# Optimization experiments

Measured on AMD Instinct MI355X. Metric: run time of the kernel, lower is better.

The kernel has to match this reference:

```python
import jax, jax.numpy as jnp
import numpy as np

B, D, H = 4096, 66, 512  # batch, system dim (22 atoms * 3), MLP hidden


def _dynamics(t, xs, W1, b1, W2, b2, W3, b3):
    # CNF vector field f(t, x): 3-layer SiLU MLP on concat([x, t])
    h = jnp.concatenate([xs, t], axis=1)          # [B, D+1]
    h = jax.nn.silu(h @ W1 + b1)                  # [B, H]
    h = jax.nn.silu(h @ W2 + b2)                  # [B, H]
    return h @ W3 + b3                            # [B, D]


def setup_inputs() -> dict:
    key = jax.random.key(0)
    ks = jax.random.split(key, 5)
    xs = jax.random.normal(ks[0], (B, D), dtype=jnp.float32)
    t = jax.random.uniform(ks[1], (B, 1), dtype=jnp.float32)
    W1 = jax.random.normal(ks[2], (D + 1, H), dtype=jnp.float32) / np.float32(np.sqrt(D + 1))
    b1 = jnp.zeros((H,), dtype=jnp.float32)
    W2 = jax.random.normal(ks[3], (H, H), dtype=jnp.float32) / np.float32(np.sqrt(H))
    b2 = jnp.zeros((H,), dtype=jnp.float32)
    W3 = jax.random.normal(ks[4], (H, D), dtype=jnp.float32) / np.float32(np.sqrt(H))
    b3 = jnp.zeros((D,), dtype=jnp.float32)
    return {"xs": xs, "t": t, "W1": W1, "b1": b1, "W2": W2, "b2": b2, "W3": W3, "b3": b3}


def reference(xs, t, W1, b1, W2, b2, W3, b3):
    # Exact divergence: trace of Jacobian d f / d x, computed with D JVPs
    # (forward-mode equivalent of the torch per-dim autograd.grad loop).
    def f(x):
        return _dynamics(t, x, W1, b1, W2, b2, W3, b3)

    dxs = f(xs)                                   # [B, D]
    eye = jnp.eye(D, dtype=xs.dtype)              # basis vectors e_i

    def jvp_col(e):
        _, tang = jax.jvp(f, (xs,), (jnp.broadcast_to(e, xs.shape),))
        return tang                               # J @ e_i, shape [B, D]

    tangs = jax.vmap(jvp_col)(eye)                # [D, B, D]
    div = jnp.einsum('dbd->b', tangs)             # sum_i (J e_i)_i = tr(J)
    return dxs, -div[:, None]
```

## Files before the change

kernel.cpp:

```cpp
#include <hip/hip_runtime.h>

#define Bn 4096
#define Dn 66
#define Hn 512

typedef __attribute__((ext_vector_type(8))) short short8;
typedef __attribute__((ext_vector_type(4))) float f32x4;

__device__ __forceinline__ unsigned short f2bf(float x) {
    union { float f; unsigned u; } v; v.f = x;
    unsigned r = v.u + 0x7fffu + ((v.u >> 16) & 1u);
    return (unsigned short)(r >> 16);
}
__device__ __forceinline__ float bf2f(unsigned short h) {
    union { float f; unsigned u; } v; v.u = ((unsigned)h) << 16; return v.f;
}


__global__ __launch_bounds__(512, 2) void k_pack(
    const float* __restrict__ W1, const float* __restrict__ W2,
    const float* __restrict__ W3,
    unsigned short* __restrict__ W2P, unsigned short* __restrict__ CmP,
    unsigned short* __restrict__ W3P)
{
    const int bid = blockIdx.x, tid = threadIdx.x;
    const int lane = tid & 63, wv = tid >> 6;

    if (bid < 64) {
        const int tix = bid*8 + wv;
        const int ks = tix & 15;
        const int n = lane & 15, kg = lane >> 4;
        const int c = (tix >> 4)*16 + n;
        const int abase = ks*32 + kg*8;
        float w2v[8], m[8];
        #pragma unroll
        for (int j = 0; j < 8; ++j) {
            w2v[j] = W2[(size_t)(abase + j)*Hn + c];
            m[j] = 0.f;
        }
        for (int i = 0; i < Dn; ++i) {
            const float w3 = W3[(size_t)c*Dn + i];
            const float4 w1a = *(const float4*)&W1[(size_t)i*Hn + abase];
            const float4 w1b = *(const float4*)&W1[(size_t)i*Hn + abase + 4];
            m[0] = fmaf(w3, w1a.x, m[0]); m[1] = fmaf(w3, w1a.y, m[1]);
            m[2] = fmaf(w3, w1a.z, m[2]); m[3] = fmaf(w3, w1a.w, m[3]);
            m[4] = fmaf(w3, w1b.x, m[4]); m[5] = fmaf(w3, w1b.y, m[5]);
            m[6] = fmaf(w3, w1b.z, m[6]); m[7] = fmaf(w3, w1b.w, m[7]);
        }
        short8 pw, pc;
        #pragma unroll
        for (int j = 0; j < 8; ++j) {
            pw[j] = (short)f2bf(w2v[j]);
            pc[j] = (short)f2bf(w2v[j] * m[j]);
        }
        const size_t off = ((size_t)tix*64 + lane)*8;
        *(short8*)&W2P[off] = pw;
        *(short8*)&CmP[off] = pc;
    } else {
        const int tix = (bid - 64)*8 + wv;
        if (tix < 80) {
            const int ks = tix & 15;
            const int n = lane & 15, kg = lane >> 4;
            const int j_out = (tix >> 4)*16 + n;
            const int abase = ks*32 + kg*8;
            short8 p;
            #pragma unroll
            for (int j = 0; j < 8; ++j)
                p[j] = (j_out < Dn) ? (short)f2bf(W3[(size_t)(abase + j)*Dn + j_out]) : (short)0;
            *(short8*)&W3P[((size_t)tix*64 + lane)*8] = p;
        }
    }
}

__global__ __launch_bounds__(512, 2) void k_main(
    const float* __restrict__ xs, const float* __restrict__ tt,
    const float* __restrict__ W1, const float* __restrict__ b1,
    const unsigned short* __restrict__ W2P, const unsigned short* __restrict__ CmP,
    const float* __restrict__ b2,
    const unsigned short* __restrict__ W3P, const float* __restrict__ b3,
    float* __restrict__ out)
{
    __shared__ __align__(16) unsigned short sA[3*8192];
    __shared__ __align__(16) unsigned short sH[8192];
    __shared__ __align__(16) unsigned short sL[8192];
    __shared__ float sX[67*16];
    __shared__ float sRed[8*16];

    const int tid = threadIdx.x, lane = tid & 63, wv = tid >> 6;
    const int rt = blockIdx.x, r0 = rt*16;
    const int n = lane & 15, kg = lane >> 4;

    for (int idx = tid; idx < 67*16; idx += 512) {
        const int i = idx >> 4, r = idx & 15;
        sX[idx] = (i < Dn) ? xs[(size_t)(r0+r)*Dn + i] : tt[r0+r];
    }
    __syncthreads();

    {
        const int rg = lane & 7, cg = lane >> 3;
        const int cA = wv*64 + cg*4, cB = cA + 32;
        float z[2][8];
        {
            const float4 bA4 = *(const float4*)&b1[cA];
            const float4 bB4 = *(const float4*)&b1[cB];
            const float bb[8] = {bA4.x,bA4.y,bA4.z,bA4.w, bB4.x,bB4.y,bB4.z,bB4.w};
            #pragma unroll
            for (int j = 0; j < 8; ++j) { z[0][j] = bb[j]; z[1][j] = bb[j]; }
        }
        for (int i = 0; i < 67; ++i) {
            const float2 xf = *(const float2*)&sX[i*16 + 2*rg];
            const float4 wA = *(const float4*)&W1[(size_t)i*Hn + cA];
            const float4 wB = *(const float4*)&W1[(size_t)i*Hn + cB];
            const float ww[8] = {wA.x,wA.y,wA.z,wA.w, wB.x,wB.y,wB.z,wB.w};
            #pragma unroll
            for (int j = 0; j < 8; ++j) {
                z[0][j] = fmaf(xf.x, ww[j], z[0][j]);
                z[1][j] = fmaf(xf.y, ww[j], z[1][j]);
            }
        }
        const int kgrp = cg >> 1, joff = (cg & 1)*4;
        #pragma unroll
        for (int rr = 0; rr < 2; ++rr) {
            const int r = 2*rg + rr;
            #pragma unroll
            for (int grp = 0; grp < 2; ++grp) {
                ushort4 phi, plo, ps;
                unsigned short* PH = (unsigned short*)&phi;
                unsigned short* PL = (unsigned short*)&plo;
                unsigned short* PS = (unsigned short*)&ps;
                #pragma unroll
                for (int j = 0; j < 4; ++j) {
                    const float zv = z[rr][grp*4 + j];
                    const float sg = 1.f / (1.f + __expf(-zv));
                    const float h  = zv * sg;
                    const float sp = sg * (1.f + zv * (1.f - sg));
                    const unsigned short hh = f2bf(h);
                    PH[j] = hh;
                    PL[j] = f2bf(h - bf2f(hh));
                    PS[j] = f2bf(sp);
                }
                const int ks = 2*wv + grp;
                const int off = (ks*64 + r + 16*kgrp)*8 + joff;
                *(ushort4*)&sA[off]          = phi;
                *(ushort4*)&sA[8192 + off]   = plo;
                *(ushort4*)&sA[16384 + off]  = ps;
            }
        }
    }
    __syncthreads();

    const int ctb = wv*4;
    f32x4 zac[4], vac[4];
    #pragma unroll
    for (int ti = 0; ti < 4; ++ti) {
        const float bz = b2[(ctb + ti)*16 + n];
        zac[ti] = (f32x4){bz, bz, bz, bz};
        vac[ti] = (f32x4){0.f, 0.f, 0.f, 0.f};
    }
    #pragma unroll 2
    for (int ks = 0; ks < 16; ++ks) {
        const int ao = (ks*64 + lane)*8;
        const short8 ahi = *(const short8*)&sA[ao];
        const short8 alo = *(const short8*)&sA[8192 + ao];
        const short8 as1 = *(const short8*)&sA[16384 + ao];
        #pragma unroll
        for (int ti = 0; ti < 4; ++ti) {
            const size_t wo = ((size_t)((ctb + ti)*16 + ks)*64 + lane)*8;
            const short8 wf = *(const short8*)&W2P[wo];
            const short8 qf = *(const short8*)&CmP[wo];
            zac[ti] = __builtin_amdgcn_mfma_f32_16x16x32_bf16(ahi, wf, zac[ti], 0, 0, 0);
            zac[ti] = __builtin_amdgcn_mfma_f32_16x16x32_bf16(alo, wf, zac[ti], 0, 0, 0);
            vac[ti] = __builtin_amdgcn_mfma_f32_16x16x32_bf16(as1, qf, vac[ti], 0, 0, 0);
        }
    }

    float dp[4] = {0.f, 0.f, 0.f, 0.f};
    #pragma unroll
    for (int ti = 0; ti < 4; ++ti) {
        const int c = (ctb + ti)*16 + n;
        const int ks2 = c >> 5, kg2 = (c >> 3) & 3, j2 = c & 7;
        #pragma unroll
        for (int q = 0; q < 4; ++q) {
            const float z2 = zac[ti][q];
            const float sg = 1.f / (1.f + __expf(-z2));
            const float h2 = z2 * sg;
            dp[q] = fmaf(sg * (1.f + z2 * (1.f - sg)), vac[ti][q], dp[q]);
            const unsigned short hh = f2bf(h2);
            const int o = (ks2*64 + (kg*4 + q) + 16*kg2)*8 + j2;
            sH[o] = hh;
            sL[o] = f2bf(h2 - bf2f(hh));
        }
    }
    #pragma unroll
    for (int q = 0; q < 4; ++q) {
        float v = dp[q];
        v += __shfl_xor(v, 1, 64);
        v += __shfl_xor(v, 2, 64);
        v += __shfl_xor(v, 4, 64);
        v += __shfl_xor(v, 8, 64);
        if (n == 0) sRed[wv*16 + kg*4 + q] = v;
    }
    __syncthreads();

    if (tid < 16) {
        float s = 0.f;
        #pragma unroll
        for (int q = 0; q < 8; ++q) s += sRed[q*16 + tid];
        out[(size_t)Bn*Dn + r0 + tid] = -s;
    }

    if (wv < 5) {
        const int jt = wv;
        const int j = jt*16 + n;
        const float bj = (j < Dn) ? b3[j] : 0.f;
        f32x4 oac = (f32x4){bj, bj, bj, bj};
        #pragma unroll 4
        for (int ks = 0; ks < 16; ++ks) {
            const int aoff = (ks*64 + lane)*8;
            const short8 ahi = *(const short8*)&sH[aoff];
            const short8 alo = *(const short8*)&sL[aoff];
            const short8 wf  = *(const short8*)&W3P[((size_t)(jt*16 + ks)*64 + lane)*8];
            oac = __builtin_amdgcn_mfma_f32_16x16x32_bf16(ahi, wf, oac, 0, 0, 0);
            oac = __builtin_amdgcn_mfma_f32_16x16x32_bf16(alo, wf, oac, 0, 0, 0);
        }
        if (j < Dn) {
            #pragma unroll
            for (int q = 0; q < 4; ++q)
                out[(size_t)(r0 + kg*4 + q)*Dn + j] = oac[q];
        }
    }
}

extern "C" void kernel_launch(void* const* d_in, const int* in_sizes, int n_in,
                              void* d_out, int out_size, void* d_ws, size_t ws_size,
                              hipStream_t stream)
{
    const float* xs = (const float*)d_in[0];
    const float* t  = (const float*)d_in[1];
    const float* W1 = (const float*)d_in[2];
    const float* b1 = (const float*)d_in[3];
    const float* W2 = (const float*)d_in[4];
    const float* b2 = (const float*)d_in[5];
    const float* W3 = (const float*)d_in[6];
    const float* b3 = (const float*)d_in[7];
    float* out = (float*)d_out;

    char* ws = (char*)d_ws;
    unsigned short* W2P = (unsigned short*)(ws);
    unsigned short* CmP = (unsigned short*)(ws + 524288);
    unsigned short* W3P = (unsigned short*)(ws + 1048576);

    k_pack<<<74,  512, 0, stream>>>(W1, W2, W3, W2P, CmP, W3P);
    k_main<<<256, 512, 0, stream>>>(xs, t, W1, b1, W2P, CmP, b2, W3P, b3, out);
}
```

Before: 118.5 us.

## Double main-kernel block to 1024 threads, reuse sA for layer-3 input, stage W3 in LDS

The main kernel now runs 16 waves per 16-row tile instead of 8. Each wave handles half as many layer-1 columns and half as many layer-2 column tiles, which spreads the per-block work over more wavefronts. The separate sH/sL shared buffers are dropped: the layer-2 outputs now overwrite sA after an added barrier, which cuts LDS use. The pack kernel stages the 16 needed W3 rows in shared memory so they are not read with strided global loads. The risks are the extra barrier and higher register pressure under launch_bounds(1024,4).

Measured after the change: 115.1 us. -2.9%, faster.

```diff
diff --git a/kernel.cpp b/kernel.cpp
--- a/kernel.cpp
+++ b/kernel.cpp
@@ -23,14 +23,23 @@
     unsigned short* __restrict__ W2P, unsigned short* __restrict__ CmP,
     unsigned short* __restrict__ W3P)
 {
+    __shared__ float sW3[16*68];
     const int bid = blockIdx.x, tid = threadIdx.x;
     const int lane = tid & 63, wv = tid >> 6;
 
     if (bid < 64) {
-        const int tix = bid*8 + wv;
-        const int ks = tix & 15;
+        const int ct = bid >> 1;
+        {
+            const int r = tid >> 5, ii = tid & 31;
+            const float* src = &W3[(size_t)(ct*16 + r)*Dn];
+            sW3[r*68 + ii] = src[ii];
+            sW3[r*68 + ii + 32] = src[ii + 32];
+            if (ii < 2) sW3[r*68 + ii + 64] = src[ii + 64];
+        }
+        __syncthreads();
+        const int ks = (bid & 1)*8 + wv;
         const int n = lane & 15, kg = lane >> 4;
-        const int c = (tix >> 4)*16 + n;
+        const int c = ct*16 + n;
         const int abase = ks*32 + kg*8;
         float w2v[8], m[8];
         #pragma unroll
@@ -38,8 +47,9 @@
             w2v[j] = W2[(size_t)(abase + j)*Hn + c];
             m[j] = 0.f;
         }
+        #pragma unroll 2
         for (int i = 0; i < Dn; ++i) {
-            const float w3 = W3[(size_t)c*Dn + i];
+            const float w3 = sW3[n*68 + i];
             const float4 w1a = *(const float4*)&W1[(size_t)i*Hn + abase];
             const float4 w1b = *(const float4*)&W1[(size_t)i*Hn + abase + 4];
             m[0] = fmaf(w3, w1a.x, m[0]); m[1] = fmaf(w3, w1a.y, m[1]);
@@ -53,7 +63,7 @@
             pw[j] = (short)f2bf(w2v[j]);
             pc[j] = (short)f2bf(w2v[j] * m[j]);
         }
-        const size_t off = ((size_t)tix*64 + lane)*8;
+        const size_t off = ((size_t)(ct*16 + ks)*64 + lane)*8;
         *(short8*)&W2P[off] = pw;
         *(short8*)&CmP[off] = pc;
     } else {
@@ -72,7 +82,7 @@
     }
 }
 
-__global__ __launch_bounds__(512, 2) void k_main(
+__global__ __launch_bounds__(1024, 4) void k_main(
     const float* __restrict__ xs, const float* __restrict__ tt,
     const float* __restrict__ W1, const float* __restrict__ b1,
     const unsigned short* __restrict__ W2P, const unsigned short* __restrict__ CmP,
@@ -81,16 +91,14 @@
     float* __restrict__ out)
 {
     __shared__ __align__(16) unsigned short sA[3*8192];
-    __shared__ __align__(16) unsigned short sH[8192];
-    __shared__ __align__(16) unsigned short sL[8192];
     __shared__ float sX[67*16];
-    __shared__ float sRed[8*16];
+    __shared__ float sRed[16*16];
 
     const int tid = threadIdx.x, lane = tid & 63, wv = tid >> 6;
     const int rt = blockIdx.x, r0 = rt*16;
     const int n = lane & 15, kg = lane >> 4;
 
-    for (int idx = tid; idx < 67*16; idx += 512) {
+    for (int idx = tid; idx < 67*16; idx += 1024) {
         const int i = idx >> 4, r = idx & 15;
         sX[idx] = (i < Dn) ? xs[(size_t)(r0+r)*Dn + i] : tt[r0+r];
     }
@@ -98,22 +106,20 @@
 
     {
         const int rg = lane & 7, cg = lane >> 3;
-        const int cA = wv*64 + cg*4, cB = cA + 32;
-        float z[2][8];
+        const int c0 = wv*32 + cg*4;
+        float z[2][4];
         {
-            const float4 bA4 = *(const float4*)&b1[cA];
-            const float4 bB4 = *(const float4*)&b1[cB];
-            const float bb[8] = {bA4.x,bA4.y,bA4.z,bA4.w, bB4.x,bB4.y,bB4.z,bB4.w};
-            #pragma unroll
-            for (int j = 0; j < 8; ++j) { z[0][j] = bb[j]; z[1][j] = bb[j]; }
-        }
+            const float4 b4 = *(const float4*)&b1[c0];
+            z[0][0]=b4.x; z[0][1]=b4.y; z[0][2]=b4.z; z[0][3]=b4.w;
+            z[1][0]=b4.x; z[1][1]=b4.y; z[1][2]=b4.z; z[1][3]=b4.w;
+        }
+        #pragma unroll 2
         for (int i = 0; i < 67; ++i) {
             const float2 xf = *(const float2*)&sX[i*16 + 2*rg];
-            const float4 wA = *(const float4*)&W1[(size_t)i*Hn + cA];
-            const float4 wB = *(const float4*)&W1[(size_t)i*Hn + cB];
-            const float ww[8] = {wA.x,wA.y,wA.z,wA.w, wB.x,wB.y,wB.z,wB.w};
-            #pragma unroll
-            for (int j = 0; j < 8; ++j) {
+            const float4 wA = *(const float4*)&W1[(size_t)i*Hn + c0];
+            const float ww[4] = {wA.x, wA.y, wA.z, wA.w};
+            #pragma unroll
+            for (int j = 0; j < 4; ++j) {
                 z[0][j] = fmaf(xf.x, ww[j], z[0][j]);
                 z[1][j] = fmaf(xf.y, ww[j], z[1][j]);
             }
@@ -122,37 +128,33 @@
         #pragma unroll
         for (int rr = 0; rr < 2; ++rr) {
             const int r = 2*rg + rr;
-            #pragma unroll
-            for (int grp = 0; grp < 2; ++grp) {
-                ushort4 phi, plo, ps;
-                unsigned short* PH = (unsigned short*)&phi;
-                unsigned short* PL = (unsigned short*)&plo;
-                unsigned short* PS = (unsigned short*)&ps;
-                #pragma unroll
-                for (int j = 0; j < 4; ++j) {
-                    const float zv = z[rr][grp*4 + j];
-                    const float sg = 1.f / (1.f + __expf(-zv));
-                    const float h  = zv * sg;
-                    const float sp = sg * (1.f + zv * (1.f - sg));
-                    const unsigned short hh = f2bf(h);
-                    PH[j] = hh;
-                    PL[j] = f2bf(h - bf2f(hh));
-                    PS[j] = f2bf(sp);
-                }
-                const int ks = 2*wv + grp;
-                const int off = (ks*64 + r + 16*kgrp)*8 + joff;
-                *(ushort4*)&sA[off]          = phi;
-                *(ushort4*)&sA[8192 + off]   = plo;
-                *(ushort4*)&sA[16384 + off]  = ps;
+            ushort4 phi, plo, ps;
+            unsigned short* PH = (unsigned short*)&phi;
+            unsigned short* PL = (unsigned short*)&plo;
+            unsigned short* PS = (unsigned short*)&ps;
+            #pragma unroll
+            for (int j = 0; j < 4; ++j) {
+                const float zv = z[rr][j];
+                const float sg = 1.f / (1.f + __expf(-zv));
+                const float h  = zv * sg;
+                const float sp = sg * (1.f + zv * (1.f - sg));
+                const unsigned short hh = f2bf(h);
+                PH[j] = hh;
+                PL[j] = f2bf(h - bf2f(hh));
+                PS[j] = f2bf(sp);
             }
-        }
-    }
-    __syncthreads();
-
-    const int ctb = wv*4;
-    f32x4 zac[4], vac[4];
+            const int off = (wv*64 + r + 16*kgrp)*8 + joff;
+            *(ushort4*)&sA[off]         = phi;
+            *(ushort4*)&sA[8192 + off]  = plo;
+            *(ushort4*)&sA[16384 + off] = ps;
+        }
+    }
+    __syncthreads();
+
+    const int ctb = wv*2;
+    f32x4 zac[2], vac[2];
     #pragma unroll
-    for (int ti = 0; ti < 4; ++ti) {
+    for (int ti = 0; ti < 2; ++ti) {
         const float bz = b2[(ctb + ti)*16 + n];
         zac[ti] = (f32x4){bz, bz, bz, bz};
         vac[ti] = (f32x4){0.f, 0.f, 0.f, 0.f};
@@ -164,7 +166,7 @@
         const short8 alo = *(const short8*)&sA[8192 + ao];
         const short8 as1 = *(const short8*)&sA[16384 + ao];
         #pragma unroll
-        for (int ti = 0; ti < 4; ++ti) {
+        for (int ti = 0; ti < 2; ++ti) {
             const size_t wo = ((size_t)((ctb + ti)*16 + ks)*64 + lane)*8;
             const short8 wf = *(const short8*)&W2P[wo];
             const short8 qf = *(const short8*)&CmP[wo];
@@ -173,10 +175,11 @@
             vac[ti] = __builtin_amdgcn_mfma_f32_16x16x32_bf16(as1, qf, vac[ti], 0, 0, 0);
         }
     }
+    __syncthreads();
 
     float dp[4] = {0.f, 0.f, 0.f, 0.f};
     #pragma unroll
-    for (int ti = 0; ti < 4; ++ti) {
+    for (int ti = 0; ti < 2; ++ti) {
         const int c = (ctb + ti)*16 + n;
         const int ks2 = c >> 5, kg2 = (c >> 3) & 3, j2 = c & 7;
         #pragma unroll
@@ -187,8 +190,8 @@
             dp[q] = fmaf(sg * (1.f + z2 * (1.f - sg)), vac[ti][q], dp[q]);
             const unsigned short hh = f2bf(h2);
             const int o = (ks2*64 + (kg*4 + q) + 16*kg2)*8 + j2;
-            sH[o] = hh;
-            sL[o] = f2bf(h2 - bf2f(hh));
+            sA[o] = hh;
+            sA[8192 + o] = f2bf(h2 - bf2f(hh));
         }
     }
     #pragma unroll
@@ -205,7 +208,7 @@
     if (tid < 16) {
         float s = 0.f;
         #pragma unroll
-        for (int q = 0; q < 8; ++q) s += sRed[q*16 + tid];
+        for (int q = 0; q < 16; ++q) s += sRed[q*16 + tid];
         out[(size_t)Bn*Dn + r0 + tid] = -s;
     }
 
@@ -217,8 +220,8 @@
         #pragma unroll 4
         for (int ks = 0; ks < 16; ++ks) {
             const int aoff = (ks*64 + lane)*8;
-            const short8 ahi = *(const short8*)&sH[aoff];
-            const short8 alo = *(const short8*)&sL[aoff];
+            const short8 ahi = *(const short8*)&sA[aoff];
+            const short8 alo = *(const short8*)&sA[8192 + aoff];
             const short8 wf  = *(const short8*)&W3P[((size_t)(jt*16 + ks)*64 + lane)*8];
             oac = __builtin_amdgcn_mfma_f32_16x16x32_bf16(ahi, wf, oac, 0, 0, 0);
             oac = __builtin_amdgcn_mfma_f32_16x16x32_bf16(alo, wf, oac, 0, 0, 0);
@@ -250,6 +253,6 @@
     unsigned short* CmP = (unsigned short*)(ws + 524288);
     unsigned short* W3P = (unsigned short*)(ws + 1048576);
 
-    k_pack<<<74,  512, 0, stream>>>(W1, W2, W3, W2P, CmP, W3P);
-    k_main<<<256, 512, 0, stream>>>(xs, t, W1, b1, W2P, CmP, b2, W3P, b3, out);
-}
+    k_pack<<<74,  512,  0, stream>>>(W1, W2, W3, W2P, CmP, W3P);
+    k_main<<<256, 1024, 0, stream>>>(xs, t, W1, b1, W2P, CmP, b2, W3P, b3, out);
+}
```
